# Performance work log

Measured on AMD Instinct MI355X. Metric: run time of the kernel, lower is better.

The kernel has to match this reference:

```python
import jax, jax.numpy as jnp
import numpy as np

E = 256      # embed_dim
H = 4        # num_heads
EXP = 4      # expansion_factor
B, C, R = 8, 32, 255  # batch, max_cols, rows (seq = R+1 with CLS)
LN_EPS = 1e-5


def setup_inputs() -> dict:
    key = jax.random.key(0)
    ks = jax.random.split(key, 16)
    s = 0.02
    return {
        "x": jax.random.normal(ks[0], (B, C, R, E), jnp.float32),
        "real_cols": jax.random.randint(ks[1], (B,), 0, C + 1),
        "real_rows": jax.random.randint(ks[2], (B,), 0, R + 1),
        "cls_token": jax.random.normal(ks[3], (E,), jnp.float32) * s,
        # MHA in_proj (torch packs q,k,v as (3E, E)) and out_proj
        "w_qkv": jax.random.normal(ks[4], (3 * E, E), jnp.float32) * s,
        "b_qkv": jnp.zeros((3 * E,), jnp.float32),
        "w_out": jax.random.normal(ks[5], (E, E), jnp.float32) * s,
        "b_out": jnp.zeros((E,), jnp.float32),
        # LayerNorm
        "ln_g": jnp.ones((E,), jnp.float32),
        "ln_b": jnp.zeros((E,), jnp.float32),
        # FFN: Linear(E, 4E) -> ReLU -> Linear(4E, E)
        "w1": jax.random.normal(ks[6], (EXP * E, E), jnp.float32) * s,
        "b1": jnp.zeros((EXP * E,), jnp.float32),
        "w2": jax.random.normal(ks[7], (E, EXP * E), jnp.float32) * s,
        "b2": jnp.zeros((E,), jnp.float32),
    }


def reference(x, real_cols, real_rows, cls_token, w_qkv, b_qkv, w_out, b_out,
              ln_g, ln_b, w1, b1, w2, b2):
    Bn, Cn, Rn, En = x.shape
    S = Rn + 1
    Dh = En // H
    dt = x.dtype

    # prepend CLS token to every column's row sequence -> (B, C, S, E)
    cls = jnp.broadcast_to(cls_token.astype(dt), (Bn, Cn, 1, En))
    xc = jnp.concatenate([cls, x], axis=2)

    # fused qkv projection
    qkv = jnp.einsum('bcse,fe->bcsf', xc, w_qkv.astype(dt)) + b_qkv.astype(dt)
    q, k, v = jnp.split(qkv, 3, axis=-1)
    q = q.reshape(Bn, Cn, S, H, Dh)
    k = k.reshape(Bn, Cn, S, H, Dh)
    v = v.reshape(Bn, Cn, S, H, Dh)

    scale = 1.0 / np.sqrt(Dh).astype(np.float32)
    scores = jnp.einsum('bcqhd,bckhd->bchqk', q, k) * scale  # (B,C,H,S,S)

    # key_padding_mask: position 0 (CLS) always valid; row p (1..R) valid iff p <= nrow
    pos = jnp.arange(S)
    valid = (pos[None, :] == 0) | (pos[None, :] <= real_rows[:, None])  # (B, S)
    neg = jnp.asarray(-1e9, scores.dtype)
    scores = jnp.where(valid[:, None, None, None, :], scores, neg)

    attn = jax.nn.softmax(scores, axis=-1)
    ctx = jnp.einsum('bchqk,bckhd->bcqhd', attn, v).reshape(Bn, Cn, S, En)
    mha = jnp.einsum('bcse,fe->bcsf', ctx, w_out.astype(dt)) + b_out.astype(dt)

    # LayerNorm over E
    mu = mha.mean(axis=-1, keepdims=True)
    var = ((mha - mu) ** 2).mean(axis=-1, keepdims=True)
    ln = (mha - mu) * jax.lax.rsqrt(var + LN_EPS) * ln_g.astype(dt) + ln_b.astype(dt)

    # FFN with residual from ln (out = ln + ffn(ln))
    h = jax.nn.relu(jnp.einsum('bcse,fe->bcsf', ln, w1.astype(dt)) + b1.astype(dt))
    ffn = jnp.einsum('bcsf,ef->bcse', h, w2.astype(dt)) + b2.astype(dt)
    out = ln + ffn

    # rep_mode == 'cls': take CLS position; zero out padded columns
    rep = out[:, :, 0, :]  # (B, C, E)
    col_valid = (jnp.arange(Cn)[None, :] < real_cols[:, None]).astype(dt)
    return rep * col_valid[..., None]
```

## Files before the change

kernel.cpp:

```cpp
#include <hip/hip_runtime.h>
#include <hip/hip_bf16.h>
#include <math.h>

static constexpr int kC = 32, kR = 255, kE = 256;

__device__ float g_q0kv[768];
__device__ float g_qw[4 * 256];
__device__ float g_s0[4];
__device__ float g_qb[4];
__device__ float g_m[256 * 4 * 4];
__device__ float g_l[256 * 4 * 4];
__device__ float g_part[256 * 4 * 4 * 256];
__device__ unsigned short g_wv_bf[256 * 256];
__device__ unsigned short g_wout_bf[256 * 256];
__device__ unsigned short g_w1_bf[1024 * 256];
__device__ unsigned short g_w2_bf[256 * 1024];

__device__ inline unsigned short f2bf(float f) {
  __hip_bfloat16 h = __float2bfloat16(f);
  return __builtin_bit_cast(unsigned short, h);
}
__device__ inline float bflo(unsigned int u) { return __uint_as_float(u << 16); }
__device__ inline float bfhi(unsigned int u) { return __uint_as_float(u & 0xffff0000u); }

__global__ __launch_bounds__(256) void k_setup(const float* __restrict__ cls,
                                               const float* __restrict__ w_qkv,
                                               const float* __restrict__ b_qkv,
                                               const float* __restrict__ w_out,
                                               const float* __restrict__ w1,
                                               const float* __restrict__ w2) {
  const int t = threadIdx.x, wvi = t >> 6, l = t & 63;

  if (blockIdx.x >= 44) {
    const int row = 512 + (blockIdx.x - 44) * 4 + wvi;
    float4 w4 = *((const float4*)(w_qkv + (size_t)row * 256) + l);
    float4 c4 = *((const float4*)cls + l);
    float a = w4.x * c4.x + w4.y * c4.y + w4.z * c4.z + w4.w * c4.w;
#pragma unroll
    for (int m = 1; m < 64; m <<= 1) a += __shfl_xor(a, m);
    if (l == 0) g_q0kv[row] = a + b_qkv[row];
    return;
  }

  if (blockIdx.x >= 4) {
    const int u = blockIdx.x - 4;
    const float* src;
    unsigned short* dst;
    int R, C, o0, e0;
    if (u < 4) { src = w_qkv + 512 * 256; dst = g_wv_bf; R = 256; C = 256; o0 = u * 64; e0 = 0; }
    else if (u < 8) { src = w_out; dst = g_wout_bf; R = 256; C = 256; o0 = (u - 4) * 64; e0 = 0; }
    else if (u < 24) { src = w1; dst = g_w1_bf; R = 1024; C = 256; o0 = (u - 8) * 64; e0 = 0; }
    else { const int v = u - 24; src = w2; dst = g_w2_bf; R = 256; C = 1024; o0 = (v >> 2) * 64; e0 = (v & 3) * 256; }

    __shared__ unsigned short tile[64 * 260];
    for (int r = wvi; r < 64; r += 4) {
      float4 v = *((const float4*)(src + (size_t)(o0 + r) * C + e0) + l);
      ushort4 ov;
      ov.x = f2bf(v.x); ov.y = f2bf(v.y); ov.z = f2bf(v.z); ov.w = f2bf(v.w);
      *(ushort4*)&tile[r * 260 + 4 * l] = ov;
    }
    __syncthreads();
    const int e80 = e0 >> 3;
    for (int e8l = wvi; e8l < 32; e8l += 4) {
      const unsigned int* tp = (const unsigned int*)&tile[l * 260 + e8l * 8];
      uint4 o;
      o.x = tp[0]; o.y = tp[1]; o.z = tp[2]; o.w = tp[3];
      *(uint4*)(dst + ((size_t)(e80 + e8l) * R + o0 + l) * 8) = o;
    }
    return;
  }

  const int h = blockIdx.x;
  __shared__ float q0h[64];
  __shared__ float kch[64];
  {
    const int r = t >> 1, half = t & 1;
    const int row = (r < 64) ? (h * 64 + r) : (256 + h * 64 + (r - 64));
    const float4* wp = (const float4*)(w_qkv + (size_t)row * 256 + half * 128);
    const float4* cp = (const float4*)cls + half * 32;
    float a = 0.f;
#pragma unroll 8
    for (int j = 0; j < 32; ++j) {
      float4 w4 = wp[j];
      float4 cv = cp[j];
      a += w4.x * cv.x + w4.y * cv.y + w4.z * cv.z + w4.w * cv.w;
    }
    a += __shfl_xor(a, 1);
    if (half == 0) {
      const float val = a + b_qkv[row];
      if (r < 64) q0h[r] = val; else kch[r - 64] = val;
    }
  }
  __syncthreads();

  float acc = 0.f;
#pragma unroll 8
  for (int j = 0; j < 64; ++j)
    acc += q0h[j] * w_qkv[(size_t)(256 + h * 64 + j) * 256 + t];
  g_qw[h * 256 + t] = acc * 0.125f;
  if (wvi == 0) {
    const float q = q0h[l];
    float pk = q * kch[l];
    float pb = q * b_qkv[256 + h * 64 + l];
#pragma unroll
    for (int m = 1; m < 64; m <<= 1) {
      pk += __shfl_xor(pk, m);
      pb += __shfl_xor(pb, m);
    }
    if (l == 0) {
      g_s0[h] = pk * 0.125f;
      g_qb[h] = pb * 0.125f;
    }
  }
}

__global__ __launch_bounds__(256) void k_attn(const float* __restrict__ x,
                                              const int* __restrict__ real_cols,
                                              const int* __restrict__ real_rows) {
  const int bc = blockIdx.x, chunk = blockIdx.y;
  const int b = bc >> 5, c = bc & 31;
  if (c >= real_cols[b]) return;
  const int rr = real_rows[b];
  const int r0 = chunk * 64;
  const int nr = min(64, rr - r0);
  if (nr <= 0) return;

  __shared__ float xs[64][260];
  __shared__ float qws[4][256];
  __shared__ float ps[4][64];
  const int t = threadIdx.x, wv = t >> 6, l = t & 63;

#pragma unroll
  for (int i = 0; i < 4; ++i) qws[i][t] = g_qw[i * 256 + t];

  const float* xb = x + ((size_t)bc * kR + r0) * kE;
  for (int r = wv; r < nr; r += 4)
    *(float4*)&xs[r][4 * l] = *(const float4*)(xb + (size_t)r * kE + 4 * l);
  __syncthreads();

  const int h = wv, row = l;
  float acc = 0.f;
  const float4* qrow = (const float4*)&qws[h][0];
  const float4* xrow = (const float4*)&xs[row][0];
#pragma unroll 8
  for (int e4 = 0; e4 < 64; ++e4) {
    float4 q4 = qrow[e4];
    float4 x4 = xrow[e4];
    acc += q4.x * x4.x + q4.y * x4.y + q4.z * x4.z + q4.w * x4.w;
  }
  float s = (row < nr) ? acc + g_qb[h] : -1e30f;
  float mx = s;
#pragma unroll
  for (int m = 1; m < 64; m <<= 1) mx = fmaxf(mx, __shfl_xor(mx, m));
  float p = (row < nr) ? __expf(s - mx) : 0.f;
  float lsum = p;
#pragma unroll
  for (int m = 1; m < 64; m <<= 1) lsum += __shfl_xor(lsum, m);
  ps[h][row] = p;
  if (l == 0) {
    g_m[(bc * 4 + chunk) * 4 + h] = mx;
    g_l[(bc * 4 + chunk) * 4 + h] = lsum;
  }
  __syncthreads();

  float a0 = 0.f, a1 = 0.f, a2 = 0.f, a3 = 0.f;
  for (int r2 = 0; r2 < nr; ++r2) {
    float xv = xs[r2][t];
    a0 += ps[0][r2] * xv;
    a1 += ps[1][r2] * xv;
    a2 += ps[2][r2] * xv;
    a3 += ps[3][r2] * xv;
  }
  float* pp = g_part + (size_t)(bc * 4 + chunk) * 4 * 256;
  pp[0 * 256 + t] = a0;
  pp[1 * 256 + t] = a1;
  pp[2 * 256 + t] = a2;
  pp[3 * 256 + t] = a3;
}

__global__ __launch_bounds__(256) void k_token(const int* __restrict__ real_cols,
                                               const int* __restrict__ real_rows,
                                               const float* __restrict__ b_qkv,
                                               const float* __restrict__ b_out,
                                               const float* __restrict__ ln_g,
                                               const float* __restrict__ ln_b,
                                               const float* __restrict__ b1,
                                               const float* __restrict__ b2,
                                               float* __restrict__ out) {
  const int bc = blockIdx.x, b = bc >> 5, c = bc & 31;
  const int t = threadIdx.x, wv = t >> 6, l = t & 63;
  if (c >= real_cols[b]) {
    out[(size_t)bc * 256 + t] = 0.f;
    return;
  }
  const int rr = real_rows[b];
  const int nch = (rr + 63) >> 6;

  __shared__ float xb[4][256];
  __shared__ float ctxs[256];
  __shared__ float lns[256];
  __shared__ float hs[1024];
  __shared__ float al[4][4];
  __shared__ float p0s[4];
  __shared__ float rb[2][4];

  if (t < 4) {
    const int h = t;
    const float s0 = g_s0[h];
    float M = s0;
    for (int ch = 0; ch < nch; ++ch) M = fmaxf(M, g_m[(bc * 4 + ch) * 4 + h]);
    float lt = __expf(s0 - M);
    const float w0 = lt;
    float av[4] = {0.f, 0.f, 0.f, 0.f};
    for (int ch = 0; ch < nch; ++ch) {
      float e = __expf(g_m[(bc * 4 + ch) * 4 + h] - M);
      av[ch] = e;
      lt += g_l[(bc * 4 + ch) * 4 + h] * e;
    }
    const float inv = 1.f / lt;
#pragma unroll
    for (int ch = 0; ch < 4; ++ch) al[h][ch] = av[ch] * inv;
    p0s[h] = w0 * inv;
  }
  __syncthreads();

#pragma unroll
  for (int h = 0; h < 4; ++h) {
    float a = 0.f;
    for (int ch = 0; ch < nch; ++ch)
      a += al[h][ch] * g_part[(size_t)(bc * 4 + ch) * 4 * 256 + h * 256 + t];
    xb[h][t] = a;
  }
  __syncthreads();

  {
    const int h = wv;
    const float p0 = p0s[h];
    float acc = p0 * g_q0kv[512 + t] + (1.f - p0) * b_qkv[512 + t];
    const uint4* wr = (const uint4*)g_wv_bf;
    const float4* v4p = (const float4*)&xb[h][0];
#pragma unroll 4
    for (int e8 = 0; e8 < 32; ++e8) {
      uint4 w = wr[e8 * 256 + t];
      float4 a = v4p[2 * e8], bb = v4p[2 * e8 + 1];
      acc += bflo(w.x) * a.x + bfhi(w.x) * a.y + bflo(w.y) * a.z + bfhi(w.y) * a.w +
             bflo(w.z) * bb.x + bfhi(w.z) * bb.y + bflo(w.w) * bb.z + bfhi(w.w) * bb.w;
    }
    ctxs[t] = acc;
  }
  __syncthreads();

  float mh;
  {
    float acc = b_out[t];
    const uint4* wr = (const uint4*)g_wout_bf;
    const float4* c4 = (const float4*)&ctxs[0];
#pragma unroll 4
    for (int e8 = 0; e8 < 32; ++e8) {
      uint4 w = wr[e8 * 256 + t];
      float4 a = c4[2 * e8], bb = c4[2 * e8 + 1];
      acc += bflo(w.x) * a.x + bfhi(w.x) * a.y + bflo(w.y) * a.z + bfhi(w.y) * a.w +
             bflo(w.z) * bb.x + bfhi(w.z) * bb.y + bflo(w.w) * bb.z + bfhi(w.w) * bb.w;
    }
    mh = acc;
  }

  float s1 = mh, s2 = mh * mh;
#pragma unroll
  for (int m = 1; m < 64; m <<= 1) {
    s1 += __shfl_xor(s1, m);
    s2 += __shfl_xor(s2, m);
  }
  if (l == 0) {
    rb[0][wv] = s1;
    rb[1][wv] = s2;
  }
  __syncthreads();
  const float mu = (rb[0][0] + rb[0][1] + rb[0][2] + rb[0][3]) * (1.f / 256.f);
  const float msq = (rb[1][0] + rb[1][1] + rb[1][2] + rb[1][3]) * (1.f / 256.f);
  const float var = msq - mu * mu;
  const float lnv = (mh - mu) * rsqrtf(var + 1e-5f) * ln_g[t] + ln_b[t];
  lns[t] = lnv;
  __syncthreads();

  {
    const uint4* wr = (const uint4*)g_w1_bf;
    float acc1[4];
#pragma unroll
    for (int k = 0; k < 4; ++k) acc1[k] = b1[t + 256 * k];
    for (int e8 = 0; e8 < 32; ++e8) {
      const float4 a = *(const float4*)&lns[8 * e8];
      const float4 bbv = *(const float4*)&lns[8 * e8 + 4];
#pragma unroll
      for (int k = 0; k < 4; ++k) {
        uint4 w = wr[e8 * 1024 + t + 256 * k];
        acc1[k] += bflo(w.x) * a.x + bfhi(w.x) * a.y + bflo(w.y) * a.z + bfhi(w.y) * a.w +
                   bflo(w.z) * bbv.x + bfhi(w.z) * bbv.y + bflo(w.w) * bbv.z + bfhi(w.w) * bbv.w;
      }
    }
#pragma unroll
    for (int k = 0; k < 4; ++k) hs[t + 256 * k] = fmaxf(acc1[k], 0.f);
  }
  __syncthreads();

  {
    const uint4* wr = (const uint4*)g_w2_bf;
    const float4* h4 = (const float4*)&hs[0];
    float acc = b2[t];
    for (int f8 = 0; f8 < 128; ++f8) {
      uint4 w = wr[f8 * 256 + t];
      float4 a = h4[2 * f8], bb = h4[2 * f8 + 1];
      acc += bflo(w.x) * a.x + bfhi(w.x) * a.y + bflo(w.y) * a.z + bfhi(w.y) * a.w +
             bflo(w.z) * bb.x + bfhi(w.z) * bb.y + bflo(w.w) * bb.z + bfhi(w.w) * bb.w;
    }
    out[(size_t)bc * 256 + t] = lnv + acc;
  }
}

extern "C" void kernel_launch(void* const* d_in, const int* in_sizes, int n_in,
                              void* d_out, int out_size, void* d_ws, size_t ws_size,
                              hipStream_t stream) {
  const float* x = (const float*)d_in[0];
  const int* real_cols = (const int*)d_in[1];
  const int* real_rows = (const int*)d_in[2];
  const float* cls = (const float*)d_in[3];
  const float* w_qkv = (const float*)d_in[4];
  const float* b_qkv = (const float*)d_in[5];
  const float* w_out = (const float*)d_in[6];
  const float* b_out = (const float*)d_in[7];
  const float* ln_g = (const float*)d_in[8];
  const float* ln_b = (const float*)d_in[9];
  const float* w1 = (const float*)d_in[10];
  const float* b1 = (const float*)d_in[11];
  const float* w2 = (const float*)d_in[12];
  const float* b2 = (const float*)d_in[13];
  float* out = (float*)d_out;
  (void)in_sizes; (void)n_in; (void)out_size; (void)d_ws; (void)ws_size;

  k_setup<<<108, 256, 0, stream>>>(cls, w_qkv, b_qkv, w_out, w1, w2);
  k_attn<<<dim3(256, 4), 256, 0, stream>>>(x, real_cols, real_rows);
  k_token<<<256, 256, 0, stream>>>(real_cols, real_rows, b_qkv, b_out, ln_g, ln_b, b1, b2, out);
}
```

Measured before the change: 177.7 us.

## Move weight conversion into attention kernel and widen token kernel to 1024 threads

The bf16 weight conversion and V-row CLS projection blocks move from the setup kernel into extra blocks of the attention grid, leaving only the 4-block head setup in the first launch. The per-column token kernel now uses 1024 threads and splits each matvec's reduction dimension four ways, with partial sums combined through shared memory. The aim is shorter serial critical paths and better latency hiding in the small token matvecs. The cost is more barriers and shared-memory traffic, plus the attention kernel's larger union shared buffer.

```diff
diff --git a/kernel.cpp b/kernel.cpp
--- a/kernel.cpp
+++ b/kernel.cpp
@@ -23,53 +23,10 @@
 __device__ inline float bflo(unsigned int u) { return __uint_as_float(u << 16); }
 __device__ inline float bfhi(unsigned int u) { return __uint_as_float(u & 0xffff0000u); }
 
-__global__ __launch_bounds__(256) void k_setup(const float* __restrict__ cls,
+__global__ __launch_bounds__(256) void k_heads(const float* __restrict__ cls,
                                                const float* __restrict__ w_qkv,
-                                               const float* __restrict__ b_qkv,
-                                               const float* __restrict__ w_out,
-                                               const float* __restrict__ w1,
-                                               const float* __restrict__ w2) {
+                                               const float* __restrict__ b_qkv) {
   const int t = threadIdx.x, wvi = t >> 6, l = t & 63;
-
-  if (blockIdx.x >= 44) {
-    const int row = 512 + (blockIdx.x - 44) * 4 + wvi;
-    float4 w4 = *((const float4*)(w_qkv + (size_t)row * 256) + l);
-    float4 c4 = *((const float4*)cls + l);
-    float a = w4.x * c4.x + w4.y * c4.y + w4.z * c4.z + w4.w * c4.w;
-#pragma unroll
-    for (int m = 1; m < 64; m <<= 1) a += __shfl_xor(a, m);
-    if (l == 0) g_q0kv[row] = a + b_qkv[row];
-    return;
-  }
-
-  if (blockIdx.x >= 4) {
-    const int u = blockIdx.x - 4;
-    const float* src;
-    unsigned short* dst;
-    int R, C, o0, e0;
-    if (u < 4) { src = w_qkv + 512 * 256; dst = g_wv_bf; R = 256; C = 256; o0 = u * 64; e0 = 0; }
-    else if (u < 8) { src = w_out; dst = g_wout_bf; R = 256; C = 256; o0 = (u - 4) * 64; e0 = 0; }
-    else if (u < 24) { src = w1; dst = g_w1_bf; R = 1024; C = 256; o0 = (u - 8) * 64; e0 = 0; }
-    else { const int v = u - 24; src = w2; dst = g_w2_bf; R = 256; C = 1024; o0 = (v >> 2) * 64; e0 = (v & 3) * 256; }
-
-    __shared__ unsigned short tile[64 * 260];
-    for (int r = wvi; r < 64; r += 4) {
-      float4 v = *((const float4*)(src + (size_t)(o0 + r) * C + e0) + l);
-      ushort4 ov;
-      ov.x = f2bf(v.x); ov.y = f2bf(v.y); ov.z = f2bf(v.z); ov.w = f2bf(v.w);
-      *(ushort4*)&tile[r * 260 + 4 * l] = ov;
-    }
-    __syncthreads();
-    const int e80 = e0 >> 3;
-    for (int e8l = wvi; e8l < 32; e8l += 4) {
-      const unsigned int* tp = (const unsigned int*)&tile[l * 260 + e8l * 8];
-      uint4 o;
-      o.x = tp[0]; o.y = tp[1]; o.z = tp[2]; o.w = tp[3];
-      *(uint4*)(dst + ((size_t)(e80 + e8l) * R + o0 + l) * 8) = o;
-    }
-    return;
-  }
-
   const int h = blockIdx.x;
   __shared__ float q0h[64];
   __shared__ float kch[64];
@@ -116,8 +73,57 @@
 
 __global__ __launch_bounds__(256) void k_attn(const float* __restrict__ x,
                                               const int* __restrict__ real_cols,
-                                              const int* __restrict__ real_rows) {
-  const int bc = blockIdx.x, chunk = blockIdx.y;
+                                              const int* __restrict__ real_rows,
+                                              const float* __restrict__ cls,
+                                              const float* __restrict__ w_qkv,
+                                              const float* __restrict__ b_qkv,
+                                              const float* __restrict__ w_out,
+                                              const float* __restrict__ w1,
+                                              const float* __restrict__ w2) {
+  const int t = threadIdx.x, wv = t >> 6, l = t & 63;
+  const int bid = blockIdx.x;
+  __shared__ __align__(16) char smem[71680];
+
+  if (bid >= 1064) {
+    const int row = 512 + (bid - 1064) * 4 + wv;
+    float4 w4 = *((const float4*)(w_qkv + (size_t)row * 256) + l);
+    float4 c4 = *((const float4*)cls + l);
+    float a = w4.x * c4.x + w4.y * c4.y + w4.z * c4.z + w4.w * c4.w;
+#pragma unroll
+    for (int m = 1; m < 64; m <<= 1) a += __shfl_xor(a, m);
+    if (l == 0) g_q0kv[row] = a + b_qkv[row];
+    return;
+  }
+
+  if (bid >= 1024) {
+    const int u = bid - 1024;
+    const float* src;
+    unsigned short* dst;
+    int R, C, o0, e0;
+    if (u < 4) { src = w_qkv + 512 * 256; dst = g_wv_bf; R = 256; C = 256; o0 = u * 64; e0 = 0; }
+    else if (u < 8) { src = w_out; dst = g_wout_bf; R = 256; C = 256; o0 = (u - 4) * 64; e0 = 0; }
+    else if (u < 24) { src = w1; dst = g_w1_bf; R = 1024; C = 256; o0 = (u - 8) * 64; e0 = 0; }
+    else { const int v = u - 24; src = w2; dst = g_w2_bf; R = 256; C = 1024; o0 = (v >> 2) * 64; e0 = (v & 3) * 256; }
+
+    unsigned short* tile = (unsigned short*)smem;
+    for (int r = wv; r < 64; r += 4) {
+      float4 v = *((const float4*)(src + (size_t)(o0 + r) * C + e0) + l);
+      ushort4 ov;
+      ov.x = f2bf(v.x); ov.y = f2bf(v.y); ov.z = f2bf(v.z); ov.w = f2bf(v.w);
+      *(ushort4*)&tile[r * 260 + 4 * l] = ov;
+    }
+    __syncthreads();
+    const int e80 = e0 >> 3;
+    for (int e8l = wv; e8l < 32; e8l += 4) {
+      const unsigned int* tp = (const unsigned int*)&tile[l * 260 + e8l * 8];
+      uint4 o;
+      o.x = tp[0]; o.y = tp[1]; o.z = tp[2]; o.w = tp[3];
+      *(uint4*)(dst + ((size_t)(e80 + e8l) * R + o0 + l) * 8) = o;
+    }
+    return;
+  }
+
+  const int bc = bid >> 2, chunk = bid & 3;
   const int b = bc >> 5, c = bc & 31;
   if (c >= real_cols[b]) return;
   const int rr = real_rows[b];
@@ -125,10 +131,9 @@
   const int nr = min(64, rr - r0);
   if (nr <= 0) return;
 
-  __shared__ float xs[64][260];
-  __shared__ float qws[4][256];
-  __shared__ float ps[4][64];
-  const int t = threadIdx.x, wv = t >> 6, l = t & 63;
+  float (*xs)[260] = (float(*)[260])smem;
+  float (*qws)[256] = (float(*)[256])(smem + 66560);
+  float (*ps)[64] = (float(*)[64])(smem + 70656);
 
 #pragma unroll
   for (int i = 0; i < 4; ++i) qws[i][t] = g_qw[i * 256 + t];
@@ -178,25 +183,26 @@
   pp[3 * 256 + t] = a3;
 }
 
-__global__ __launch_bounds__(256) void k_token(const int* __restrict__ real_cols,
-                                               const int* __restrict__ real_rows,
-                                               const float* __restrict__ b_qkv,
-                                               const float* __restrict__ b_out,
-                                               const float* __restrict__ ln_g,
-                                               const float* __restrict__ ln_b,
-                                               const float* __restrict__ b1,
-                                               const float* __restrict__ b2,
-                                               float* __restrict__ out) {
+__global__ __launch_bounds__(1024) void k_token(const int* __restrict__ real_cols,
+                                                const int* __restrict__ real_rows,
+                                                const float* __restrict__ b_qkv,
+                                                const float* __restrict__ b_out,
+                                                const float* __restrict__ ln_g,
+                                                const float* __restrict__ ln_b,
+                                                const float* __restrict__ b1,
+                                                const float* __restrict__ b2,
+                                                float* __restrict__ out) {
   const int bc = blockIdx.x, b = bc >> 5, c = bc & 31;
   const int t = threadIdx.x, wv = t >> 6, l = t & 63;
   if (c >= real_cols[b]) {
-    out[(size_t)bc * 256 + t] = 0.f;
+    if (t < 256) out[(size_t)bc * 256 + t] = 0.f;
     return;
   }
   const int rr = real_rows[b];
   const int nch = (rr + 63) >> 6;
 
   __shared__ float xb[4][256];
+  __shared__ float part[4][256];
   __shared__ float ctxs[256];
   __shared__ float lns[256];
   __shared__ float hs[1024];
@@ -224,97 +230,112 @@
   }
   __syncthreads();
 
-#pragma unroll
-  for (int h = 0; h < 4; ++h) {
+  {
+    const int h = t >> 8, e = t & 255;
     float a = 0.f;
     for (int ch = 0; ch < nch; ++ch)
-      a += al[h][ch] * g_part[(size_t)(bc * 4 + ch) * 4 * 256 + h * 256 + t];
-    xb[h][t] = a;
-  }
-  __syncthreads();
-
-  {
-    const int h = wv;
-    const float p0 = p0s[h];
-    float acc = p0 * g_q0kv[512 + t] + (1.f - p0) * b_qkv[512 + t];
+      a += al[h][ch] * g_part[(size_t)(bc * 4 + ch) * 4 * 256 + h * 256 + e];
+    xb[h][e] = a;
+  }
+  __syncthreads();
+
+  {
+    const int f = t & 255, q = t >> 8, h = f >> 6;
     const uint4* wr = (const uint4*)g_wv_bf;
     const float4* v4p = (const float4*)&xb[h][0];
-#pragma unroll 4
-    for (int e8 = 0; e8 < 32; ++e8) {
-      uint4 w = wr[e8 * 256 + t];
+    float acc = 0.f;
+#pragma unroll
+    for (int i = 0; i < 8; ++i) {
+      const int e8 = q * 8 + i;
+      uint4 w = wr[e8 * 256 + f];
       float4 a = v4p[2 * e8], bb = v4p[2 * e8 + 1];
       acc += bflo(w.x) * a.x + bfhi(w.x) * a.y + bflo(w.y) * a.z + bfhi(w.y) * a.w +
              bflo(w.z) * bb.x + bfhi(w.z) * bb.y + bflo(w.w) * bb.z + bfhi(w.w) * bb.w;
     }
-    ctxs[t] = acc;
-  }
-  __syncthreads();
-
-  float mh;
-  {
-    float acc = b_out[t];
+    part[q][f] = acc;
+  }
+  __syncthreads();
+  if (t < 256) {
+    const int h = t >> 6;
+    const float p0 = p0s[h];
+    ctxs[t] = part[0][t] + part[1][t] + part[2][t] + part[3][t] +
+              p0 * g_q0kv[512 + t] + (1.f - p0) * b_qkv[512 + t];
+  }
+  __syncthreads();
+
+  {
+    const int g = t & 255, q = t >> 8;
     const uint4* wr = (const uint4*)g_wout_bf;
     const float4* c4 = (const float4*)&ctxs[0];
-#pragma unroll 4
-    for (int e8 = 0; e8 < 32; ++e8) {
-      uint4 w = wr[e8 * 256 + t];
+    float acc = 0.f;
+#pragma unroll
+    for (int i = 0; i < 8; ++i) {
+      const int e8 = q * 8 + i;
+      uint4 w = wr[e8 * 256 + g];
       float4 a = c4[2 * e8], bb = c4[2 * e8 + 1];
       acc += bflo(w.x) * a.x + bfhi(w.x) * a.y + bflo(w.y) * a.z + bfhi(w.y) * a.w +
              bflo(w.z) * bb.x + bfhi(w.z) * bb.y + bflo(w.w) * bb.z + bfhi(w.w) * bb.w;
     }
-    mh = acc;
-  }
-
-  float s1 = mh, s2 = mh * mh;
-#pragma unroll
-  for (int m = 1; m < 64; m <<= 1) {
-    s1 += __shfl_xor(s1, m);
-    s2 += __shfl_xor(s2, m);
-  }
-  if (l == 0) {
-    rb[0][wv] = s1;
-    rb[1][wv] = s2;
-  }
-  __syncthreads();
-  const float mu = (rb[0][0] + rb[0][1] + rb[0][2] + rb[0][3]) * (1.f / 256.f);
-  const float msq = (rb[1][0] + rb[1][1] + rb[1][2] + rb[1][3]) * (1.f / 256.f);
-  const float var = msq - mu * mu;
-  const float lnv = (mh - mu) * rsqrtf(var + 1e-5f) * ln_g[t] + ln_b[t];
-  lns[t] = lnv;
+    part[q][g] = acc;
+  }
+  __syncthreads();
+  float mh = 0.f;
+  if (t < 256) {
+    mh = part[0][t] + part[1][t] + part[2][t] + part[3][t] + b_out[t];
+    float s1 = mh, s2 = mh * mh;
+#pragma unroll
+    for (int m = 1; m < 64; m <<= 1) {
+      s1 += __shfl_xor(s1, m);
+      s2 += __shfl_xor(s2, m);
+    }
+    if (l == 0) {
+      rb[0][wv] = s1;
+      rb[1][wv] = s2;
+    }
+  }
+  __syncthreads();
+  if (t < 256) {
+    const float mu = (rb[0][0] + rb[0][1] + rb[0][2] + rb[0][3]) * (1.f / 256.f);
+    const float msq = (rb[1][0] + rb[1][1] + rb[1][2] + rb[1][3]) * (1.f / 256.f);
+    const float var = msq - mu * mu;
+    lns[t] = (mh - mu) * rsqrtf(var + 1e-5f) * ln_g[t] + ln_b[t];
+  }
   __syncthreads();
 
   {
     const uint4* wr = (const uint4*)g_w1_bf;
-    float acc1[4];
-#pragma unroll
-    for (int k = 0; k < 4; ++k) acc1[k] = b1[t + 256 * k];
+    float acc = b1[t];
+#pragma unroll
     for (int e8 = 0; e8 < 32; ++e8) {
+      uint4 w = wr[e8 * 1024 + t];
       const float4 a = *(const float4*)&lns[8 * e8];
       const float4 bbv = *(const float4*)&lns[8 * e8 + 4];
-#pragma unroll
-      for (int k = 0; k < 4; ++k) {
-        uint4 w = wr[e8 * 1024 + t + 256 * k];
-        acc1[k] += bflo(w.x) * a.x + bfhi(w.x) * a.y + bflo(w.y) * a.z + bfhi(w.y) * a.w +
-                   bflo(w.z) * bbv.x + bfhi(w.z) * bbv.y + bflo(w.w) * bbv.z + bfhi(w.w) * bbv.w;
-      }
-    }
-#pragma unroll
-    for (int k = 0; k < 4; ++k) hs[t + 256 * k] = fmaxf(acc1[k], 0.f);
-  }
-  __syncthreads();
-
-  {
+      acc += bflo(w.x) * a.x + bfhi(w.x) * a.y + bflo(w.y) * a.z + bfhi(w.y) * a.w +
+             bflo(w.z) * bbv.x + bfhi(w.z) * bbv.y + bflo(w.w) * bbv.z + bfhi(w.w) * bbv.w;
+    }
+    hs[t] = fmaxf(acc, 0.f);
+  }
+  __syncthreads();
+
+  {
+    const int e = t & 255, q = t >> 8;
     const uint4* wr = (const uint4*)g_w2_bf;
     const float4* h4 = (const float4*)&hs[0];
-    float acc = b2[t];
-    for (int f8 = 0; f8 < 128; ++f8) {
-      uint4 w = wr[f8 * 256 + t];
+    float acc = 0.f;
+#pragma unroll 8
+    for (int i = 0; i < 32; ++i) {
+      const int f8 = q * 32 + i;
+      uint4 w = wr[f8 * 256 + e];
       float4 a = h4[2 * f8], bb = h4[2 * f8 + 1];
       acc += bflo(w.x) * a.x + bfhi(w.x) * a.y + bflo(w.y) * a.z + bfhi(w.y) * a.w +
              bflo(w.z) * bb.x + bfhi(w.z) * bb.y + bflo(w.w) * bb.z + bfhi(w.w) * bb.w;
     }
-    out[(size_t)bc * 256 + t] = lnv + acc;
-  }
+    part[q][e] = acc;
+  }
+  __syncthreads();
+  if (t < 256)
+    out[(size_t)bc * 256 + t] =
+        lns[t] + part[0][t] + part[1][t] + part[2][t] + part[3][t] + b2[t];
 }
 
 extern "C" void kernel_launch(void* const* d_in, const int* in_sizes, int n_in,
@@ -337,7 +358,7 @@
   float* out = (float*)d_out;
   (void)in_sizes; (void)n_in; (void)out_size; (void)d_ws; (void)ws_size;
 
-  k_setup<<<108, 256, 0, stream>>>(cls, w_qkv, b_qkv, w_out, w1, w2);
-  k_attn<<<dim3(256, 4), 256, 0, stream>>>(x, real_cols, real_rows);
-  k_token<<<256, 256, 0, stream>>>(real_cols, real_rows, b_qkv, b_out, ln_g, ln_b, b1, b2, out);
-}
+  k_heads<<<4, 256, 0, stream>>>(cls, w_qkv, b_qkv);
+  k_attn<<<1128, 256, 0, stream>>>(x, real_cols, real_rows, cls, w_qkv, b_qkv, w_out, w1, w2);
+  k_token<<<256, 1024, 0, stream>>>(real_cols, real_rows, b_qkv, b_out, ln_g, ln_b, b1, b2, out);
+}
```

Result: faster. 154.7 us (-12.9%).
